# Kernel tuning notes

Hardware: AMD Instinct MI355X
Metric: run time of the kernel (lower is better)

The kernel has to match this reference:

```python
import jax, jax.numpy as jnp
import numpy as np

NEG_SLOPE = 0.2  # PyG GATConv default


def gat_conv(x, src, dst, W, att_src, att_dst, bias, num_nodes, concat):
    """Faithful PyG GATConv forward (self-loops assumed already added).
    x: [N, F_in]; src/dst: [E]; W: [F_in, H*C]; att_src/att_dst: [H, C]."""
    H, C = att_src.shape
    h = (x @ W).reshape(num_nodes, H, C)                      # [N, H, C]
    a_src = (h * att_src[None]).sum(-1)                       # [N, H]
    a_dst = (h * att_dst[None]).sum(-1)                       # [N, H]
    alpha = jax.nn.leaky_relu(a_src[src] + a_dst[dst], NEG_SLOPE)  # [E, H]
    # segment softmax over incoming edges of each dst node (numerically stable)
    m = jax.ops.segment_max(alpha, dst, num_segments=num_nodes)    # [N, H]
    e = jnp.exp(alpha - m[dst])                                    # [E, H]
    denom = jax.ops.segment_sum(e, dst, num_segments=num_nodes)    # [N, H]
    w = e / jnp.maximum(denom[dst], 1e-16)                         # [E, H]
    msg = h[src] * w[:, :, None]                                   # [E, H, C]
    out = jax.ops.segment_sum(msg, dst, num_segments=num_nodes)    # [N, H, C]
    out = out.reshape(num_nodes, H * C) if concat else out.mean(axis=1)
    return out + bias


def setup_inputs() -> dict:
    key = jax.random.key(0)
    ks = jax.random.split(key, 16)
    N, E, n_drones = 100000, 1600000, 10000
    IN, HID, OUT, HEADS = 6, 64, 2, 4

    x = jax.random.normal(ks[0], (N, IN), dtype=jnp.float32)
    # first n_drones nodes are drones (x[:,5] == 1.0), rest 0.0
    x = x.at[:, 5].set((jnp.arange(N) < n_drones).astype(jnp.float32))
    edge_index = jax.random.randint(ks[1], (2, E), 0, N, dtype=jnp.int64)

    s = 0.1
    params = {
        "W1": jax.random.normal(ks[2], (IN, HEADS * HID), jnp.float32) * s,
        "att_src1": jax.random.normal(ks[3], (HEADS, HID), jnp.float32) * s,
        "att_dst1": jax.random.normal(ks[4], (HEADS, HID), jnp.float32) * s,
        "b1": jax.random.normal(ks[5], (HEADS * HID,), jnp.float32) * s,
        "W2": jax.random.normal(ks[6], (HEADS * HID, HID), jnp.float32) * s,
        "att_src2": jax.random.normal(ks[7], (1, HID), jnp.float32) * s,
        "att_dst2": jax.random.normal(ks[8], (1, HID), jnp.float32) * s,
        "b2": jax.random.normal(ks[9], (HID,), jnp.float32) * s,
        "fc1_w": jax.random.normal(ks[10], (HID, 64), jnp.float32) * s,
        "fc1_b": jax.random.normal(ks[11], (64,), jnp.float32) * s,
        "fc2_w": jax.random.normal(ks[12], (64, OUT), jnp.float32) * s,
        "fc2_b": jax.random.normal(ks[13], (OUT,), jnp.float32) * s,
    }
    return {"x": x, "edge_index": edge_index, "n_drones": n_drones, **params}


def reference(x, edge_index, n_drones, W1, att_src1, att_dst1, b1,
              W2, att_src2, att_dst2, b2, fc1_w, fc1_b, fc2_w, fc2_b):
    N = x.shape[0]
    action_scale = 2.0
    # add self loops (PyG GATConv default add_self_loops=True)
    loop = jnp.arange(N, dtype=edge_index.dtype)
    src = jnp.concatenate([edge_index[0], loop])
    dst = jnp.concatenate([edge_index[1], loop])

    h = jax.nn.elu(gat_conv(x, src, dst, W1, att_src1, att_dst1, b1, N, concat=True))
    h = jax.nn.elu(gat_conv(h, src, dst, W2, att_src2, att_dst2, b2, N, concat=False))

    drone_idx = jnp.nonzero(x[:, 5] == 1.0, size=n_drones)[0]
    h_drones = h[drone_idx]                                   # [n_drones, HID]
    out = jnp.tanh(jax.nn.relu(h_drones @ fc1_w + fc1_b) @ fc2_w + fc2_b)
    return out * action_scale
```

## Files before the change

kernel.cpp:

```cpp
#include <hip/hip_runtime.h>
#include <hip/hip_fp16.h>
#include <math.h>

#define CAP 48
#define PARTBITS 8
#define BINW 256
#define NB 240
#define SEGCAP 48

typedef float f32x4 __attribute__((ext_vector_type(4)));
typedef __bf16 bf16x8 __attribute__((ext_vector_type(8)));
typedef unsigned short ushort8 __attribute__((ext_vector_type(8)));
typedef unsigned short ushort4v __attribute__((ext_vector_type(4)));
typedef int i32x4 __attribute__((ext_vector_type(4)));

__device__ __forceinline__ float leaky(float x){ return x > 0.f ? x : 0.2f * x; }
__device__ __forceinline__ float eluf(float x){ return x > 0.f ? x : __expf(x) - 1.f; }
__device__ __forceinline__ unsigned short f2bf(float f){
  unsigned u = __float_as_uint(f);
  u += 0x7FFF + ((u >> 16) & 1);
  return (unsigned short)(u >> 16);
}
__device__ __forceinline__ float bf2f(unsigned short u){
  return __uint_as_float(((unsigned)u) << 16);
}
__device__ __forceinline__ unsigned short f2h(float f){
  return __half_as_ushort(__float2half(f));
}
__device__ __forceinline__ float h2f(unsigned short u){
  return __half2float(__ushort_as_half(u));
}

__global__ __launch_bounds__(256) void k12a(const float* __restrict__ x,
    const float* __restrict__ W1, const float* __restrict__ as1,
    const float* __restrict__ ad1, const float* __restrict__ W2,
    unsigned short* __restrict__ Bfrag, ushort8* __restrict__ recA,
    ushort8* __restrict__ recB, ushort4v* __restrict__ recC,
    int* __restrict__ gtail, int N, int nbk1,
    const int* __restrict__ ei, int E, int NR,
    unsigned* __restrict__ queue, int* __restrict__ qcnt){
  __shared__ float vw[48];
  __shared__ int lcnt[512];
  int t = threadIdx.x;
  if ((int)blockIdx.x < nbk1){
    int gid = blockIdx.x * 256 + t;
    if (gid == 0) *gtail = 0;
    if (gid < 16384){
      int j  = gid & 7;
      int L  = (gid >> 3) & 63;
      int ct = (gid >> 9) & 3;
      int ks = gid >> 11;
      int k = ks*32 + ((L >> 4) & 3)*8 + j;
      int c = ct*16 + (L & 15);
      Bfrag[gid] = f2bf(W2[k*64 + c]);
    }
    if (t < 48){
      int side = t / 24, r = t % 24, f = r / 4, h = r % 4;
      const float* att = side ? ad1 : as1;
      float s = 0.f;
      for (int c = 0; c < 64; ++c) s += W1[f*256 + h*64 + c] * att[h*64 + c];
      vw[side*24 + f*4 + h] = s;
    }
    __syncthreads();
    int n = gid;
    if (n >= N) return;
    float xf[6];
    for (int f = 0; f < 6; ++f) xf[f] = x[n*6 + f];
    float as[4], ad[4];
    for (int h = 0; h < 4; ++h){
      float s = 0.f, d = 0.f;
      for (int f = 0; f < 6; ++f){ s += xf[f] * vw[f*4 + h]; d += xf[f] * vw[24 + f*4 + h]; }
      as[h] = s; ad[h] = d;
    }
    ushort8 va, vb;
    va[0]=f2bf(xf[0]); va[1]=f2bf(xf[1]); va[2]=f2bf(xf[2]); va[3]=f2bf(xf[3]);
    va[4]=f2bf(xf[4]); va[5]=f2bf(xf[5]); va[6]=f2h(as[0]); va[7]=f2h(as[1]);
    vb = va; vb[6]=f2h(as[2]); vb[7]=f2h(as[3]);
    ushort4v vc = {f2h(ad[0]), f2h(ad[1]), f2h(ad[2]), f2h(ad[3])};
    recA[n] = va;
    recB[n] = vb;
    recC[n] = vc;
  } else {
    int blk = blockIdx.x - nbk1;
    for (int i = t; i < NR; i += 256) lcnt[i] = 0;
    __syncthreads();
    int E4 = E >> 2;
    const i32x4* s4 = (const i32x4*)ei;
    const i32x4* d4 = (const i32x4*)(ei + E);
    for (int i = blk*256 + t; i < E4; i += NB*256){
      i32x4 s = __builtin_nontemporal_load(s4 + i);
      i32x4 d = __builtin_nontemporal_load(d4 + i);
      #pragma unroll
      for (int j = 0; j < 4; ++j){
        int p = d[j] >> PARTBITS;
        int r = atomicAdd(&lcnt[p], 1);
        if (r < SEGCAP){
          unsigned v = ((unsigned)s[j] << 8) | ((unsigned)d[j] & 255u);
          queue[((size_t)p*NB + blk)*SEGCAP + r] = v;
        }
      }
    }
    if (blk == 0 && t < (E & 3)){
      int e = E4*4 + t;
      int dd = ei[E + e], ss = ei[e];
      int p = dd >> PARTBITS;
      int r = atomicAdd(&lcnt[p], 1);
      if (r < SEGCAP){
        unsigned v = ((unsigned)ss << 8) | ((unsigned)dd & 255u);
        queue[((size_t)p*NB + blk)*SEGCAP + r] = v;
      }
    }
    __syncthreads();
    for (int i = t; i < NR; i += 256) qcnt[(size_t)i*NB + blk] = lcnt[i];
  }
}

__global__ __launch_bounds__(1024) void k2b34(const unsigned* __restrict__ queue,
    const int* __restrict__ qcnt,
    const ushort8* __restrict__ recA, const ushort8* __restrict__ recB,
    const ushort4v* __restrict__ recC,
    int* __restrict__ cnt, int* __restrict__ row_start,
    int* __restrict__ bucket, int* __restrict__ gtail,
    const float* __restrict__ W1, const float* __restrict__ b1,
    const unsigned short* __restrict__ Bfrag,
    const float* __restrict__ as2v, const float* __restrict__ ad2v,
    unsigned short* __restrict__ h2h, float* __restrict__ a2s,
    float* __restrict__ a2d, int nd_bins, int N){
  __shared__ int lc[BINW];
  __shared__ int scan[BINW];
  __shared__ int gbase_s;
  __shared__ union {
    int lbuck[BINW*CAP];
    struct { float w1s[6*256]; float b1s[256]; ushort8 bfs[2048]; } d;
  } u;
  __shared__ unsigned short afs[BINW*24];
  int t = threadIdx.x, bin = blockIdx.x;
  if (t < BINW) lc[t] = 0;
  __syncthreads();
  {
    int seg = t >> 2;
    if (seg < NB){
      int lq = min(qcnt[(size_t)bin*NB + seg], SEGCAP);
      const unsigned* qs = queue + ((size_t)bin*NB + seg)*SEGCAP;
      for (int j = t & 3; j < lq; j += 4){
        unsigned pr = qs[j];
        int ld = (int)(pr & 255u);
        int pos = atomicAdd(&lc[ld], 1);
        if (pos < CAP) u.lbuck[ld*CAP + pos] = (int)(pr >> 8);
      }
    }
  }
  __syncthreads();
  if (bin < nd_bins){
    if (t < 256) scan[t] = min(lc[t], CAP);
    __syncthreads();
    for (int off = 1; off < 256; off <<= 1){
      int v = 0;
      if (t < 256 && t >= off) v = scan[t - off];
      __syncthreads();
      if (t < 256) scan[t] += v;
      __syncthreads();
    }
    if (t == 0) gbase_s = atomicAdd(gtail, scan[255]);
    __syncthreads();
    int gbase = gbase_s;
    int Vn = scan[255];
    for (int vi = t; vi < Vn; vi += 1024){
      int lo = 0, hi = 255;
      while (lo < hi){ int mid = (lo+hi) >> 1; if (scan[mid] <= vi) lo = mid+1; else hi = mid; }
      int base0 = lo ? scan[lo-1] : 0;
      bucket[gbase + vi] = u.lbuck[lo*CAP + (vi - base0)];
    }
    if (t < BINW){
      cnt[bin*BINW + t] = min(lc[t], CAP);
      row_start[bin*BINW + t] = gbase + (t ? scan[t-1] : 0);
    }
    __syncthreads();
  }
  {
    int dl = t >> 2, h = t & 3;
    int n = bin*BINW + dl;
    int hp = h >> 1;
    int hi = h & 1;
    unsigned short* ob = &afs[dl*24 + h*6];
    if (n < N){
      const ushort8* R = hp ? recB : recA;
      ushort8 v0 = R[n];
      float xf[6] = {bf2f(v0[0]), bf2f(v0[1]), bf2f(v0[2]), bf2f(v0[3]), bf2f(v0[4]), bf2f(v0[5])};
      float a_s = h2f(v0[6 + hi]);
      ushort4v cc = recC[n];
      float a_d = h2f(cc[h]);
      float e0 = __expf(leaky(a_s + a_d));
      float den = e0;
      float acc[6];
      #pragma unroll
      for (int f = 0; f < 6; ++f) acc[f] = e0 * xf[f];
      int deg = min(lc[dl], CAP);
      const int* bk = &u.lbuck[dl*CAP];
      int i = 0;
      for (; i + 4 <= deg; i += 4){
        int sid[4];
        #pragma unroll
        for (int j = 0; j < 4; ++j) sid[j] = bk[i+j];
        ushort8 r[4];
        #pragma unroll
        for (int j = 0; j < 4; ++j) r[j] = R[sid[j]];
        #pragma unroll
        for (int j = 0; j < 4; ++j){
          float e = __expf(leaky(h2f(r[j][6 + hi]) + a_d));
          den += e;
          #pragma unroll
          for (int f = 0; f < 6; ++f) acc[f] += e * bf2f(r[j][f]);
        }
      }
      for (; i < deg; ++i){
        ushort8 r = R[bk[i]];
        float e = __expf(leaky(h2f(r[6 + hi]) + a_d));
        den += e;
        #pragma unroll
        for (int f = 0; f < 6; ++f) acc[f] += e * bf2f(r[f]);
      }
      float dinv = 1.f / den;
      ob[0] = f2h(acc[0]*dinv); ob[1] = f2h(acc[1]*dinv);
      ob[2] = f2h(acc[2]*dinv); ob[3] = f2h(acc[3]*dinv);
      ob[4] = f2h(acc[4]*dinv); ob[5] = f2h(acc[5]*dinv);
    } else {
      #pragma unroll
      for (int j = 0; j < 6; ++j) ob[j] = 0;
    }
  }
  __syncthreads();
  {
    const float4* w1g = (const float4*)W1;
    float4* w1l = (float4*)u.d.w1s;
    for (int i = t; i < 384; i += 1024) w1l[i] = w1g[i];
    if (t < 64) ((float4*)u.d.b1s)[t] = ((const float4*)b1)[t];
    const ushort8* bfg = (const ushort8*)Bfrag;
    #pragma unroll
    for (int i = 0; i < 2; ++i) u.d.bfs[t + 1024*i] = bfg[t + 1024*i];
  }
  __syncthreads();
  {
    int grp = t >> 8;
    int t2  = t & 255;
    int L = t2 & 63;
    int w = t2 >> 6;
    int m = L & 15;
    int quad = L >> 4;
    int base = bin*BINW + grp*64;
    int nl = grp*64 + w*16 + m;
    ushort8 u0 = *(const ushort8*)(afs + nl*24);
    ushort8 u1 = *(const ushort8*)(afs + nl*24 + 8);
    ushort8 u2 = *(const ushort8*)(afs + nl*24 + 16);
    f32x4 acc[4];
    #pragma unroll
    for (int ct = 0; ct < 4; ++ct) acc[ct] = (f32x4){0.f, 0.f, 0.f, 0.f};
    #pragma unroll
    for (int ks = 0; ks < 8; ++ks){
      int kb = ks*32 + quad*8;
      int kc = kb >> 6;
      float4 bb0 = *(const float4*)(u.d.b1s + kb);
      float4 bb1 = *(const float4*)(u.d.b1s + kb + 4);
      float s0=bb0.x, s1=bb0.y, s2=bb0.z, s3=bb0.w;
      float s4=bb1.x, s5=bb1.y, s6=bb1.z, s7=bb1.w;
      #pragma unroll
      for (int f = 0; f < 6; ++f){
        int e = kc*6 + f;
        unsigned short ah = (e < 8) ? u0[e] : ((e < 16) ? u1[e-8] : u2[e-16]);
        float a = h2f(ah);
        float4 w0 = *(const float4*)(u.d.w1s + f*256 + kb);
        float4 w1 = *(const float4*)(u.d.w1s + f*256 + kb + 4);
        s0 += a*w0.x; s1 += a*w0.y; s2 += a*w0.z; s3 += a*w0.w;
        s4 += a*w1.x; s5 += a*w1.y; s6 += a*w1.z; s7 += a*w1.w;
      }
      ushort8 ap;
      ap[0]=f2bf(eluf(s0)); ap[1]=f2bf(eluf(s1)); ap[2]=f2bf(eluf(s2)); ap[3]=f2bf(eluf(s3));
      ap[4]=f2bf(eluf(s4)); ap[5]=f2bf(eluf(s5)); ap[6]=f2bf(eluf(s6)); ap[7]=f2bf(eluf(s7));
      bf16x8 av = __builtin_bit_cast(bf16x8, ap);
      #pragma unroll
      for (int ct = 0; ct < 4; ++ct){
        bf16x8 bv = __builtin_bit_cast(bf16x8, u.d.bfs[(ks*4 + ct)*64 + L]);
        acc[ct] = __builtin_amdgcn_mfma_f32_16x16x32_bf16(av, bv, acc[ct], 0, 0, 0);
      }
    }
    float asv[4], adv[4];
    #pragma unroll
    for (int ct = 0; ct < 4; ++ct){ asv[ct] = as2v[ct*16 + m]; adv[ct] = ad2v[ct*16 + m]; }
    float ps[4] = {0,0,0,0}, pd[4] = {0,0,0,0};
    #pragma unroll
    for (int ct = 0; ct < 4; ++ct)
      #pragma unroll
      for (int r = 0; r < 4; ++r){
        ps[r] += acc[ct][r] * asv[ct];
        pd[r] += acc[ct][r] * adv[ct];
      }
    #pragma unroll
    for (int r = 0; r < 4; ++r){
      int nr = base + w*16 + quad*4 + r;
      if (nr < N){
        #pragma unroll
        for (int ct = 0; ct < 4; ++ct)
          h2h[(size_t)nr*64 + ct*16 + m] = f2h(acc[ct][r]);
      }
    }
    #pragma unroll
    for (int mask = 1; mask <= 8; mask <<= 1){
      #pragma unroll
      for (int r = 0; r < 4; ++r){
        ps[r] += __shfl_xor(ps[r], mask, 64);
        pd[r] += __shfl_xor(pd[r], mask, 64);
      }
    }
    if (m == 0){
      #pragma unroll
      for (int r = 0; r < 4; ++r){
        int nr = base + w*16 + quad*4 + r;
        if (nr < N){ a2s[nr] = ps[r]; a2d[nr] = pd[r]; }
      }
    }
  }
}

__global__ __launch_bounds__(256) void k5_out(
    const unsigned short* __restrict__ h2h, const float* __restrict__ a2s,
    const float* __restrict__ a2d, const int* __restrict__ cnt,
    const int* __restrict__ row_start, const int* __restrict__ bucket,
    const float* __restrict__ b2, const float* __restrict__ fc1w,
    const float* __restrict__ fc1b, const float* __restrict__ fc2w,
    const float* __restrict__ fc2b, float* __restrict__ out, int ND){
  __shared__ float hb[4][64];
  int lane = threadIdx.x & 63;
  int w = threadIdx.x >> 6;
  int n = blockIdx.x * 4 + w;
  if (n >= ND) return;
  float adv = a2d[n];
  float e0 = __expf(leaky(a2s[n] + adv));
  float den = e0;
  float acc = e0 * h2f(h2h[(size_t)n*64 + lane]);
  int deg = cnt[n];
  const int* bk = bucket + row_start[n];
  int i = 0;
  for (; i + 4 <= deg; i += 4){
    int sid[4];
    #pragma unroll
    for (int j = 0; j < 4; ++j) sid[j] = bk[i+j];
    float av[4]; unsigned short hv4[4];
    #pragma unroll
    for (int j = 0; j < 4; ++j){
      av[j] = a2s[sid[j]];
      hv4[j] = h2h[(size_t)sid[j]*64 + lane];
    }
    #pragma unroll
    for (int j = 0; j < 4; ++j){
      float e = __expf(leaky(av[j] + adv));
      den += e;
      acc += e * h2f(hv4[j]);
    }
  }
  for (; i < deg; ++i){
    int s = bk[i];
    float e = __expf(leaky(a2s[s] + adv));
    den += e;
    acc += e * h2f(h2h[(size_t)s*64 + lane]);
  }
  float hv = eluf(acc / den + b2[lane]);
  hb[w][lane] = hv;
  float t1 = fc1b[lane];
  for (int k = 0; k < 64; ++k) t1 += hb[w][k] * fc1w[k*64 + lane];
  t1 = fmaxf(t1, 0.f);
  float p0 = t1 * fc2w[lane*2 + 0];
  float p1 = t1 * fc2w[lane*2 + 1];
  for (int o = 32; o > 0; o >>= 1){
    p0 += __shfl_down(p0, o, 64);
    p1 += __shfl_down(p1, o, 64);
  }
  if (lane == 0){
    out[n*2 + 0] = tanhf(p0 + fc2b[0]) * 2.f;
    out[n*2 + 1] = tanhf(p1 + fc2b[1]) * 2.f;
  }
}

extern "C" void kernel_launch(void* const* d_in, const int* in_sizes, int n_in,
                              void* d_out, int out_size, void* d_ws, size_t ws_size,
                              hipStream_t stream){
  const float* x    = (const float*)d_in[0];
  const int*   ei   = (const int*)d_in[1];
  const float* W1   = (const float*)d_in[3];
  const float* as1  = (const float*)d_in[4];
  const float* ad1  = (const float*)d_in[5];
  const float* b1   = (const float*)d_in[6];
  const float* W2   = (const float*)d_in[7];
  const float* as2  = (const float*)d_in[8];
  const float* ad2  = (const float*)d_in[9];
  const float* b2   = (const float*)d_in[10];
  const float* fc1w = (const float*)d_in[11];
  const float* fc1b = (const float*)d_in[12];
  const float* fc2w = (const float*)d_in[13];
  const float* fc2b = (const float*)d_in[14];
  float* out = (float*)d_out;

  int N  = in_sizes[0] / 6;
  int E  = in_sizes[1] / 2;
  int ND = out_size / 2;
  int NR = (N + BINW - 1) >> PARTBITS;
  int nd_bins = (ND + BINW - 1) / BINW;
  int nbk1 = (N + 255) / 256;

  char* p = (char*)d_ws;
  auto alloc = [&](size_t bytes){ void* r = (void*)p; p += (bytes + 255) & ~(size_t)255; return r; };
  int*            cnt    = (int*)           alloc((size_t)NR * BINW * 4);
  int*            rowst  = (int*)           alloc((size_t)NR * BINW * 4);
  int*            bucket = (int*)           alloc(((size_t)E + 1024) * 4);
  ushort8*        recA   = (ushort8*)       alloc((size_t)N * 16);
  ushort8*        recB   = (ushort8*)       alloc((size_t)N * 16);
  ushort4v*       recC   = (ushort4v*)      alloc((size_t)N * 8);
  unsigned short* h2h    = (unsigned short*)alloc((size_t)N * 128);
  float*          a2s    = (float*)         alloc((size_t)N * 4);
  float*          a2d    = (float*)         alloc((size_t)N * 4);
  unsigned short* Bfrag  = (unsigned short*)alloc(16384 * 2);
  unsigned*       queue  = (unsigned*)      alloc((size_t)NR * NB * SEGCAP * 4);
  int*            qcnt   = (int*)           alloc((size_t)NR * NB * 4);
  int*            gtail  = (int*)           alloc(256);

  size_t needed = (size_t)(p - (char*)d_ws);
  if (needed > ws_size) return;

  k12a<<<nbk1 + NB, 256, 0, stream>>>(x, W1, as1, ad1, W2, Bfrag, recA, recB,
                                      recC, gtail, N, nbk1, ei, E, NR, queue, qcnt);
  k2b34<<<NR, 1024, 0, stream>>>(queue, qcnt, recA, recB, recC,
                                 cnt, rowst, bucket, gtail,
                                 W1, b1, Bfrag, as2, ad2,
                                 h2h, a2s, a2d, nd_bins, N);
  k5_out<<<(ND + 3)/4, 256, 0, stream>>>(h2h, a2s, a2d, cnt, rowst, bucket, b2,
                                         fc1w, fc1b, fc2w, fc2b, out, ND);
}
```

Measured before the change: 175.9 us.

## Replace two-pass partitioned CSR build with direct global-atomic fixed-capacity buckets

Replaces the partition queue plus per-bin LDS regroup and scan-based compaction with direct per-destination global atomicAdd into a fixed CAP-slot bucket array. This drops the queue write/read pass, the shared-memory scan and the row_start indirection. The fused layer kernel now runs with 128-node tiles and 512 threads, reading neighbor lists from global memory. In exchange it issues about 1.6M global atomics with scattered writes, adds a memset, and uses a larger padded bucket array.

```diff
diff --git a/kernel.cpp b/kernel.cpp
--- a/kernel.cpp
+++ b/kernel.cpp
@@ -3,10 +3,8 @@
 #include <math.h>
 
 #define CAP 48
-#define PARTBITS 8
-#define BINW 256
-#define NB 240
-#define SEGCAP 48
+#define NB 512
+#define TILE 128
 
 typedef float f32x4 __attribute__((ext_vector_type(4)));
 typedef __bf16 bf16x8 __attribute__((ext_vector_type(8)));
@@ -36,15 +34,12 @@
     const float* __restrict__ ad1, const float* __restrict__ W2,
     unsigned short* __restrict__ Bfrag, ushort8* __restrict__ recA,
     ushort8* __restrict__ recB, ushort4v* __restrict__ recC,
-    int* __restrict__ gtail, int N, int nbk1,
-    const int* __restrict__ ei, int E, int NR,
-    unsigned* __restrict__ queue, int* __restrict__ qcnt){
+    int N, int nbk1, const int* __restrict__ ei, int E,
+    int* __restrict__ cnt, int* __restrict__ bucket){
   __shared__ float vw[48];
-  __shared__ int lcnt[512];
   int t = threadIdx.x;
   if ((int)blockIdx.x < nbk1){
     int gid = blockIdx.x * 256 + t;
-    if (gid == 0) *gtail = 0;
     if (gid < 16384){
       int j  = gid & 7;
       int L  = (gid >> 3) & 63;
@@ -82,104 +77,52 @@
     recC[n] = vc;
   } else {
     int blk = blockIdx.x - nbk1;
-    for (int i = t; i < NR; i += 256) lcnt[i] = 0;
-    __syncthreads();
     int E4 = E >> 2;
     const i32x4* s4 = (const i32x4*)ei;
     const i32x4* d4 = (const i32x4*)(ei + E);
     for (int i = blk*256 + t; i < E4; i += NB*256){
       i32x4 s = __builtin_nontemporal_load(s4 + i);
       i32x4 d = __builtin_nontemporal_load(d4 + i);
-      #pragma unroll
-      for (int j = 0; j < 4; ++j){
-        int p = d[j] >> PARTBITS;
-        int r = atomicAdd(&lcnt[p], 1);
-        if (r < SEGCAP){
-          unsigned v = ((unsigned)s[j] << 8) | ((unsigned)d[j] & 255u);
-          queue[((size_t)p*NB + blk)*SEGCAP + r] = v;
-        }
-      }
+      int pos[4];
+      #pragma unroll
+      for (int j = 0; j < 4; ++j) pos[j] = atomicAdd(&cnt[d[j]], 1);
+      #pragma unroll
+      for (int j = 0; j < 4; ++j)
+        if (pos[j] < CAP) bucket[(size_t)d[j]*CAP + pos[j]] = s[j];
     }
     if (blk == 0 && t < (E & 3)){
       int e = E4*4 + t;
       int dd = ei[E + e], ss = ei[e];
-      int p = dd >> PARTBITS;
-      int r = atomicAdd(&lcnt[p], 1);
-      if (r < SEGCAP){
-        unsigned v = ((unsigned)ss << 8) | ((unsigned)dd & 255u);
-        queue[((size_t)p*NB + blk)*SEGCAP + r] = v;
-      }
-    }
-    __syncthreads();
-    for (int i = t; i < NR; i += 256) qcnt[(size_t)i*NB + blk] = lcnt[i];
-  }
-}
-
-__global__ __launch_bounds__(1024) void k2b34(const unsigned* __restrict__ queue,
-    const int* __restrict__ qcnt,
+      int pos = atomicAdd(&cnt[dd], 1);
+      if (pos < CAP) bucket[(size_t)dd*CAP + pos] = ss;
+    }
+  }
+}
+
+__global__ __launch_bounds__(512) void k34(
+    const int* __restrict__ cnt, const int* __restrict__ bucket,
     const ushort8* __restrict__ recA, const ushort8* __restrict__ recB,
     const ushort4v* __restrict__ recC,
-    int* __restrict__ cnt, int* __restrict__ row_start,
-    int* __restrict__ bucket, int* __restrict__ gtail,
     const float* __restrict__ W1, const float* __restrict__ b1,
     const unsigned short* __restrict__ Bfrag,
     const float* __restrict__ as2v, const float* __restrict__ ad2v,
     unsigned short* __restrict__ h2h, float* __restrict__ a2s,
-    float* __restrict__ a2d, int nd_bins, int N){
-  __shared__ int lc[BINW];
-  __shared__ int scan[BINW];
-  __shared__ int gbase_s;
-  __shared__ union {
-    int lbuck[BINW*CAP];
-    struct { float w1s[6*256]; float b1s[256]; ushort8 bfs[2048]; } d;
-  } u;
-  __shared__ unsigned short afs[BINW*24];
-  int t = threadIdx.x, bin = blockIdx.x;
-  if (t < BINW) lc[t] = 0;
-  __syncthreads();
+    float* __restrict__ a2d, int N){
+  __shared__ float w1s[6*256];
+  __shared__ float b1s[256];
+  __shared__ ushort8 bfs[2048];
+  __shared__ unsigned short afs[TILE*24];
+  int t = threadIdx.x, blk = blockIdx.x;
   {
-    int seg = t >> 2;
-    if (seg < NB){
-      int lq = min(qcnt[(size_t)bin*NB + seg], SEGCAP);
-      const unsigned* qs = queue + ((size_t)bin*NB + seg)*SEGCAP;
-      for (int j = t & 3; j < lq; j += 4){
-        unsigned pr = qs[j];
-        int ld = (int)(pr & 255u);
-        int pos = atomicAdd(&lc[ld], 1);
-        if (pos < CAP) u.lbuck[ld*CAP + pos] = (int)(pr >> 8);
-      }
-    }
-  }
-  __syncthreads();
-  if (bin < nd_bins){
-    if (t < 256) scan[t] = min(lc[t], CAP);
-    __syncthreads();
-    for (int off = 1; off < 256; off <<= 1){
-      int v = 0;
-      if (t < 256 && t >= off) v = scan[t - off];
-      __syncthreads();
-      if (t < 256) scan[t] += v;
-      __syncthreads();
-    }
-    if (t == 0) gbase_s = atomicAdd(gtail, scan[255]);
-    __syncthreads();
-    int gbase = gbase_s;
-    int Vn = scan[255];
-    for (int vi = t; vi < Vn; vi += 1024){
-      int lo = 0, hi = 255;
-      while (lo < hi){ int mid = (lo+hi) >> 1; if (scan[mid] <= vi) lo = mid+1; else hi = mid; }
-      int base0 = lo ? scan[lo-1] : 0;
-      bucket[gbase + vi] = u.lbuck[lo*CAP + (vi - base0)];
-    }
-    if (t < BINW){
-      cnt[bin*BINW + t] = min(lc[t], CAP);
-      row_start[bin*BINW + t] = gbase + (t ? scan[t-1] : 0);
-    }
-    __syncthreads();
+    if (t < 384) ((float4*)w1s)[t] = ((const float4*)W1)[t];
+    if (t < 64) ((float4*)b1s)[t] = ((const float4*)b1)[t];
+    const ushort8* bfg = (const ushort8*)Bfrag;
+    #pragma unroll
+    for (int i = 0; i < 4; ++i) bfs[t + 512*i] = bfg[t + 512*i];
   }
   {
     int dl = t >> 2, h = t & 3;
-    int n = bin*BINW + dl;
+    int n = blk*TILE + dl;
     int hp = h >> 1;
     int hi = h & 1;
     unsigned short* ob = &afs[dl*24 + h*6];
@@ -195,8 +138,8 @@
       float acc[6];
       #pragma unroll
       for (int f = 0; f < 6; ++f) acc[f] = e0 * xf[f];
-      int deg = min(lc[dl], CAP);
-      const int* bk = &u.lbuck[dl*CAP];
+      int deg = min(cnt[n], CAP);
+      const int* bk = bucket + (size_t)n*CAP;
       int i = 0;
       for (; i + 4 <= deg; i += 4){
         int sid[4];
@@ -228,16 +171,6 @@
       #pragma unroll
       for (int j = 0; j < 6; ++j) ob[j] = 0;
     }
-  }
-  __syncthreads();
-  {
-    const float4* w1g = (const float4*)W1;
-    float4* w1l = (float4*)u.d.w1s;
-    for (int i = t; i < 384; i += 1024) w1l[i] = w1g[i];
-    if (t < 64) ((float4*)u.d.b1s)[t] = ((const float4*)b1)[t];
-    const ushort8* bfg = (const ushort8*)Bfrag;
-    #pragma unroll
-    for (int i = 0; i < 2; ++i) u.d.bfs[t + 1024*i] = bfg[t + 1024*i];
   }
   __syncthreads();
   {
@@ -247,7 +180,7 @@
     int w = t2 >> 6;
     int m = L & 15;
     int quad = L >> 4;
-    int base = bin*BINW + grp*64;
+    int base = blk*TILE + grp*64;
     int nl = grp*64 + w*16 + m;
     ushort8 u0 = *(const ushort8*)(afs + nl*24);
     ushort8 u1 = *(const ushort8*)(afs + nl*24 + 8);
@@ -259,8 +192,8 @@
     for (int ks = 0; ks < 8; ++ks){
       int kb = ks*32 + quad*8;
       int kc = kb >> 6;
-      float4 bb0 = *(const float4*)(u.d.b1s + kb);
-      float4 bb1 = *(const float4*)(u.d.b1s + kb + 4);
+      float4 bb0 = *(const float4*)(b1s + kb);
+      float4 bb1 = *(const float4*)(b1s + kb + 4);
       float s0=bb0.x, s1=bb0.y, s2=bb0.z, s3=bb0.w;
       float s4=bb1.x, s5=bb1.y, s6=bb1.z, s7=bb1.w;
       #pragma unroll
@@ -268,8 +201,8 @@
         int e = kc*6 + f;
         unsigned short ah = (e < 8) ? u0[e] : ((e < 16) ? u1[e-8] : u2[e-16]);
         float a = h2f(ah);
-        float4 w0 = *(const float4*)(u.d.w1s + f*256 + kb);
-        float4 w1 = *(const float4*)(u.d.w1s + f*256 + kb + 4);
+        float4 w0 = *(const float4*)(w1s + f*256 + kb);
+        float4 w1 = *(const float4*)(w1s + f*256 + kb + 4);
         s0 += a*w0.x; s1 += a*w0.y; s2 += a*w0.z; s3 += a*w0.w;
         s4 += a*w1.x; s5 += a*w1.y; s6 += a*w1.z; s7 += a*w1.w;
       }
@@ -279,7 +212,7 @@
       bf16x8 av = __builtin_bit_cast(bf16x8, ap);
       #pragma unroll
       for (int ct = 0; ct < 4; ++ct){
-        bf16x8 bv = __builtin_bit_cast(bf16x8, u.d.bfs[(ks*4 + ct)*64 + L]);
+        bf16x8 bv = __builtin_bit_cast(bf16x8, bfs[(ks*4 + ct)*64 + L]);
         acc[ct] = __builtin_amdgcn_mfma_f32_16x16x32_bf16(av, bv, acc[ct], 0, 0, 0);
       }
     }
@@ -324,7 +257,7 @@
 __global__ __launch_bounds__(256) void k5_out(
     const unsigned short* __restrict__ h2h, const float* __restrict__ a2s,
     const float* __restrict__ a2d, const int* __restrict__ cnt,
-    const int* __restrict__ row_start, const int* __restrict__ bucket,
+    const int* __restrict__ bucket,
     const float* __restrict__ b2, const float* __restrict__ fc1w,
     const float* __restrict__ fc1b, const float* __restrict__ fc2w,
     const float* __restrict__ fc2b, float* __restrict__ out, int ND){
@@ -337,8 +270,8 @@
   float e0 = __expf(leaky(a2s[n] + adv));
   float den = e0;
   float acc = e0 * h2f(h2h[(size_t)n*64 + lane]);
-  int deg = cnt[n];
-  const int* bk = bucket + row_start[n];
+  int deg = min(cnt[n], CAP);
+  const int* bk = bucket + (size_t)n*CAP;
   int i = 0;
   for (; i + 4 <= deg; i += 4){
     int sid[4];
@@ -402,15 +335,14 @@
   int N  = in_sizes[0] / 6;
   int E  = in_sizes[1] / 2;
   int ND = out_size / 2;
-  int NR = (N + BINW - 1) >> PARTBITS;
-  int nd_bins = (ND + BINW - 1) / BINW;
   int nbk1 = (N + 255) / 256;
+  int ntile = (N + TILE - 1) / TILE;
+  int NC = ntile * TILE;
 
   char* p = (char*)d_ws;
   auto alloc = [&](size_t bytes){ void* r = (void*)p; p += (bytes + 255) & ~(size_t)255; return r; };
-  int*            cnt    = (int*)           alloc((size_t)NR * BINW * 4);
-  int*            rowst  = (int*)           alloc((size_t)NR * BINW * 4);
-  int*            bucket = (int*)           alloc(((size_t)E + 1024) * 4);
+  int*            cnt    = (int*)           alloc((size_t)NC * 4);
+  int*            bucket = (int*)           alloc((size_t)NC * CAP * 4);
   ushort8*        recA   = (ushort8*)       alloc((size_t)N * 16);
   ushort8*        recB   = (ushort8*)       alloc((size_t)N * 16);
   ushort4v*       recC   = (ushort4v*)      alloc((size_t)N * 8);
@@ -418,19 +350,16 @@
   float*          a2s    = (float*)         alloc((size_t)N * 4);
   float*          a2d    = (float*)         alloc((size_t)N * 4);
   unsigned short* Bfrag  = (unsigned short*)alloc(16384 * 2);
-  unsigned*       queue  = (unsigned*)      alloc((size_t)NR * NB * SEGCAP * 4);
-  int*            qcnt   = (int*)           alloc((size_t)NR * NB * 4);
-  int*            gtail  = (int*)           alloc(256);
 
   size_t needed = (size_t)(p - (char*)d_ws);
   if (needed > ws_size) return;
 
+  hipMemsetAsync(cnt, 0, (size_t)NC * 4, stream);
   k12a<<<nbk1 + NB, 256, 0, stream>>>(x, W1, as1, ad1, W2, Bfrag, recA, recB,
-                                      recC, gtail, N, nbk1, ei, E, NR, queue, qcnt);
-  k2b34<<<NR, 1024, 0, stream>>>(queue, qcnt, recA, recB, recC,
-                                 cnt, rowst, bucket, gtail,
+                                      recC, N, nbk1, ei, E, cnt, bucket);
+  k34<<<ntile, 512, 0, stream>>>(cnt, bucket, recA, recB, recC,
                                  W1, b1, Bfrag, as2, ad2,
-                                 h2h, a2s, a2d, nd_bins, N);
-  k5_out<<<(ND + 3)/4, 256, 0, stream>>>(h2h, a2s, a2d, cnt, rowst, bucket, b2,
+                                 h2h, a2s, a2d, N);
+  k5_out<<<(ND + 3)/4, 256, 0, stream>>>(h2h, a2s, a2d, cnt, bucket, b2,
                                          fc1w, fc1b, fc2w, fc2b, out, ND);
 }
```

After: 268.0 us. +52.3%, slower.
